# Kernel optimization log

Measured on AMD Instinct MI355X. Metric: run time of the kernel, lower is better.

Reference implementation:

```python
import jax, jax.numpy as jnp
import numpy as np

L = 2          # conv layers
N = 50000      # nodes
E = 800000     # edges (before self loops)
F_IN = 256     # raw node features
C = 32         # embed features (out_channels per head)
H = 4          # heads
HC = H * C
ED = 1         # edge feature dim
EPS = 1e-5
NEG_SLOPE = 0.2


def _xavier(k, shape):
    fan_in, fan_out = shape[-2], shape[-1]
    lim = float(np.sqrt(6.0 / (fan_in + fan_out)))
    return jax.random.uniform(k, shape, jnp.float32, -lim, lim)


def setup_inputs() -> dict:
    key = jax.random.key(0)
    ks = jax.random.split(key, 12)
    x = jax.random.normal(ks[0], (N, F_IN), jnp.float32)
    src = jax.random.randint(ks[1], (E,), 0, N, dtype=jnp.int32)
    off = jax.random.randint(ks[2], (E,), 1, N, dtype=jnp.int32)
    dst = (src + off) % N  # guarantees no pre-existing self loops (PyG removes then re-adds them)
    edge_index = jnp.stack([src, dst])
    edge_attr = jax.random.normal(ks[3], (E, ED), jnp.float32)
    return {
        "x": x,
        "edge_index": edge_index,
        "edge_attr": edge_attr,
        "W_emb": _xavier(ks[4], (F_IN, C)),
        "b_emb": jnp.zeros((C,), jnp.float32),
        "ln0_w": jnp.ones((C,), jnp.float32),
        "ln0_b": jnp.zeros((C,), jnp.float32),
        "Wl": _xavier(ks[5], (L, C, HC)),
        "bl": jnp.zeros((L, HC), jnp.float32),
        "Wr": _xavier(ks[6], (L, C, HC)),
        "br": jnp.zeros((L, HC), jnp.float32),
        "We": _xavier(ks[7], (L, ED, HC)),
        "att": jax.random.normal(ks[8], (L, H, C), jnp.float32) * 0.1,
        "gat_b": jnp.zeros((L, HC), jnp.float32),
        "ln1_w": jnp.ones((L, HC), jnp.float32),
        "ln1_b": jnp.zeros((L, HC), jnp.float32),
        "lin_w": _xavier(ks[9], (L, HC, C)),
        "lin_b": jnp.zeros((L, C), jnp.float32),
        "ln2_w": jnp.ones((L, C), jnp.float32),
        "ln2_b": jnp.zeros((L, C), jnp.float32),
    }


def _node_ln(x, w, b):
    # torch.nn.LayerNorm over last dim
    mu = jnp.mean(x, axis=-1, keepdims=True)
    xc = x - mu
    var = jnp.mean(xc * xc, axis=-1, keepdims=True)
    return xc / jnp.sqrt(var + EPS) * w + b


def _graph_ln(x, w, b):
    # torch_geometric.nn.norm.LayerNorm, mode='graph': normalize over ALL nodes+features
    mu = jnp.mean(x)
    xc = x - mu
    var = jnp.mean(xc * xc)
    return xc / jnp.sqrt(var + EPS) * w + b


def _gatv2_layer(h, src, dst, ea, Wl, bl, Wr, br, We, att, gat_b):
    n = h.shape[0]
    xl = (h @ Wl + bl).reshape(n, H, C)   # lin_l(x) -> source transform
    xr = (h @ Wr + br).reshape(n, H, C)   # lin_r(x) -> target transform
    e = (ea @ We).reshape(-1, H, C)       # lin_edge(edge_attr), no bias
    z = jax.nn.leaky_relu(xl[src] + xr[dst] + e, NEG_SLOPE)   # [Etot,H,C]
    logits = jnp.einsum("ehc,hc->eh", z, att)                  # [Etot,H]
    # segment softmax over destination nodes (every node has a self loop)
    m = jax.ops.segment_max(logits, dst, num_segments=n)
    ex = jnp.exp(logits - m[dst])
    s = jax.ops.segment_sum(ex, dst, num_segments=n)
    alpha = ex / s[dst]                                        # [Etot,H]
    msg = alpha[..., None] * xl[src]                           # [Etot,H,C]
    out = jax.ops.segment_sum(msg, dst, num_segments=n)        # [N,H,C]
    return out.reshape(n, HC) + gat_b


def reference(x, edge_index, edge_attr, W_emb, b_emb, ln0_w, ln0_b, Wl, bl, Wr, br,
              We, att, gat_b, ln1_w, ln1_b, lin_w, lin_b, ln2_w, ln2_b):
    n = x.shape[0]
    loop = jnp.arange(n, dtype=edge_index.dtype)
    src = jnp.concatenate([edge_index[0], loop])
    dst = jnp.concatenate([edge_index[1], loop])
    ea = jnp.concatenate([edge_attr, jnp.zeros((n, edge_attr.shape[1]), edge_attr.dtype)])  # fill_value=0.0

    # node_embed: Dropout(eval=identity) -> Linear -> LayerNorm -> ReLU
    h = jax.nn.relu(_node_ln(x @ W_emb + b_emb, ln0_w, ln0_b))
    hs = [h]
    for i in range(L):
        g = _gatv2_layer(h, src, dst, ea, Wl[i], bl[i], Wr[i], br[i], We[i], att[i], gat_b[i])
        g = jax.nn.relu(_graph_ln(g, ln1_w[i], ln1_b[i]))     # PyG graph-mode LayerNorm + ReLU
        g = g @ lin_w[i] + lin_b[i]                            # heads>1 projection back to C
        h = jax.nn.relu(_node_ln(g, ln2_w[i], ln2_b[i]))
        hs.append(h)
    # JumpingKnowledge mode='max': elementwise max over layer outputs
    return jnp.max(jnp.stack(hs, axis=0), axis=0)
```

## Files before the change

### kernel.cpp

```cpp
#include <hip/hip_runtime.h>
#include <hip/hip_fp16.h>

constexpr int kNodes = 50000;
constexpr int kNE    = 800000;
constexpr int kFin   = 256;
constexpr int kC     = 32;
constexpr int kH     = 4;
constexpr int kHC    = 128;
constexpr int kTN    = 16;
constexpr int kLWP   = 130;
constexpr int kEmbedBlocks = kNodes / kTN;
constexpr int kTransBlocks = (kNodes + 31) / 32;
constexpr int kHistGS = 256;
constexpr int kReoGS  = 256;
constexpr float kEps   = 1e-5f;
constexpr float kSlope = 0.2f;
constexpr float kL2E   = 1.44269504f;
constexpr float kShift2 = 8.0f * 1.44269504f;

typedef _Float16 f16;
typedef _Float16 f16x2 __attribute__((ext_vector_type(2)));
struct alignas(16) h8 { f16x2 v[4]; };

__device__ __forceinline__ float fdot2_(f16x2 a, f16x2 b, float c) {
#if __has_builtin(__builtin_amdgcn_fdot2)
    return __builtin_amdgcn_fdot2(a, b, c, false);
#else
    return fmaf((float)a.x, (float)b.x, fmaf((float)a.y, (float)b.y, c));
#endif
}

template<int CTRL>
__device__ __forceinline__ float dpp_add(float v) {
    int x = __builtin_amdgcn_update_dpp(0, __float_as_int(v), CTRL, 0xF, 0xF, true);
    return v + __int_as_float(x);
}
__device__ __forceinline__ float red8(float p) {
    p = dpp_add<0xB1>(p);
    p = dpp_add<0x4E>(p);
    p = dpp_add<0x141>(p);
    return p;
}

__global__ void __launch_bounds__(256) k_fill0(unsigned* __restrict__ p, int n) {
    int i = blockIdx.x * 256 + threadIdx.x;
    if (i < n) p[i] = 0u;
}

__global__ void __launch_bounds__(256) k_embed_hist(
    const float* __restrict__ x, const float* __restrict__ W, const float* __restrict__ b,
    const float* __restrict__ lnw, const float* __restrict__ lnb,
    float* __restrict__ h, float* __restrict__ jk,
    const int* __restrict__ dst, int* __restrict__ deg, unsigned short* __restrict__ rank) {
    __shared__ f16 sxh[kTN * kFin];
    __shared__ f16 sWh[kFin / 8 * kC * 8];
    int t = threadIdx.x;
    if (blockIdx.x < kHistGS) {
        const int stride = kHistGS * 256;
        int e = blockIdx.x * 256 + t;
        for (; e + 3 * stride < kNE; e += 4 * stride) {
            int d0 = dst[e], d1 = dst[e + stride], d2 = dst[e + 2 * stride], d3 = dst[e + 3 * stride];
            int r0 = atomicAdd(&deg[d0], 1);
            int r1 = atomicAdd(&deg[d1], 1);
            int r2 = atomicAdd(&deg[d2], 1);
            int r3 = atomicAdd(&deg[d3], 1);
            rank[e] = (unsigned short)r0;
            rank[e + stride] = (unsigned short)r1;
            rank[e + 2 * stride] = (unsigned short)r2;
            rank[e + 3 * stride] = (unsigned short)r3;
        }
        for (; e < kNE; e += stride) {
            int d = dst[e];
            rank[e] = (unsigned short)atomicAdd(&deg[d], 1);
        }
        return;
    }
    int n0 = (blockIdx.x - kHistGS) * kTN;
    for (int i = t; i < kFin * kC; i += 256) {
        int k = i >> 5, c = i & 31;
        sWh[((k >> 3) * kC + c) * 8 + (k & 7)] = (f16)W[i];
    }
    const float2* xg2 = (const float2*)(x + (long)n0 * kFin);
    f16x2* sx2 = (f16x2*)sxh;
    for (int i = t; i < kTN * kFin / 2; i += 256) {
        float2 v = xg2[i];
        f16x2 hv; hv.x = (f16)v.x; hv.y = (f16)v.y;
        sx2[i] = hv;
    }
    __syncthreads();
    int c = t & 31, n2 = t >> 5;
    const h8* xa = (const h8*)(sxh + n2 * kFin);
    const h8* xb = (const h8*)(sxh + (n2 + 8) * kFin);
    const h8* wr = (const h8*)sWh;
    float a0 = 0.f, a0b = 0.f, a1 = 0.f, a1b = 0.f;
    #pragma unroll 8
    for (int i8 = 0; i8 < kFin / 8; ++i8) {
        h8 xv0 = xa[i8];
        h8 xv1 = xb[i8];
        h8 wv  = wr[i8 * kC + c];
        a0  = fdot2_(xv0.v[0], wv.v[0], a0);
        a0b = fdot2_(xv0.v[1], wv.v[1], a0b);
        a0  = fdot2_(xv0.v[2], wv.v[2], a0);
        a0b = fdot2_(xv0.v[3], wv.v[3], a0b);
        a1  = fdot2_(xv1.v[0], wv.v[0], a1);
        a1b = fdot2_(xv1.v[1], wv.v[1], a1b);
        a1  = fdot2_(xv1.v[2], wv.v[2], a1);
        a1b = fdot2_(xv1.v[3], wv.v[3], a1b);
    }
    float acc0 = a0 + a0b, acc1 = a1 + a1b;
    float bc = b[c], lw = lnw[c], lb = lnb[c];
    {
        float y = acc0 + bc;
        float m = y;
        #pragma unroll
        for (int o = 1; o < 32; o <<= 1) m += __shfl_xor(m, o);
        m *= (1.f / kC);
        float xc = y - m, v = xc * xc;
        #pragma unroll
        for (int o = 1; o < 32; o <<= 1) v += __shfl_xor(v, o);
        v *= (1.f / kC);
        float out = fmaxf(xc * rsqrtf(v + kEps) * lw + lb, 0.f);
        int node = n0 + n2;
        h[node * kC + c] = out;
        jk[node * kC + c] = out;
    }
    {
        float y = acc1 + bc;
        float m = y;
        #pragma unroll
        for (int o = 1; o < 32; o <<= 1) m += __shfl_xor(m, o);
        m *= (1.f / kC);
        float xc = y - m, v = xc * xc;
        #pragma unroll
        for (int o = 1; o < 32; o <<= 1) v += __shfl_xor(v, o);
        v *= (1.f / kC);
        float out = fmaxf(xc * rsqrtf(v + kEps) * lw + lb, 0.f);
        int node = n0 + n2 + 8;
        h[node * kC + c] = out;
        jk[node * kC + c] = out;
    }
}

__device__ __forceinline__ void trans_body(
    int bid, float* s_h, const float* __restrict__ h,
    const float* __restrict__ Wl, const float* __restrict__ bl,
    const float* __restrict__ Wr, const float* __restrict__ br,
    __half* __restrict__ xl, float* __restrict__ xr) {
    int t = threadIdx.x;
    int j = t & 127, hf = t >> 7;
    float wl[kC], wr[kC];
    #pragma unroll
    for (int k = 0; k < kC; ++k) { wl[k] = Wl[k * kHC + j]; wr[k] = Wr[k * kHC + j]; }
    float blj = bl[j], brj = br[j];
    int n0 = bid * 32;
    int nn = min(32, kNodes - n0);
    for (int i = t; i < nn * kC; i += 256) s_h[i] = h[n0 * kC + i];
    __syncthreads();
    int nend = min(nn, hf * 16 + 16);
    for (int n = hf * 16; n < nend; ++n) {
        const float4* h4 = (const float4*)(s_h + n * kC);
        float al = blj, ar = brj;
        #pragma unroll
        for (int kq = 0; kq < 8; ++kq) {
            float4 hv = h4[kq];
            al += hv.x * wl[kq*4] + hv.y * wl[kq*4+1] + hv.z * wl[kq*4+2] + hv.w * wl[kq*4+3];
            ar += hv.x * wr[kq*4] + hv.y * wr[kq*4+1] + hv.z * wr[kq*4+2] + hv.w * wr[kq*4+3];
        }
        long g = (long)(n0 + n) * kHC + j;
        xl[g] = __float2half(al);
        xr[g] = ar;
    }
}

__global__ void __launch_bounds__(256) k_trans(
    const float* __restrict__ h,
    const float* __restrict__ Wl, const float* __restrict__ bl,
    const float* __restrict__ Wr, const float* __restrict__ br,
    __half* __restrict__ xl, float* __restrict__ xr) {
    __shared__ float s_h[32 * kC];
    trans_body(blockIdx.x, s_h, h, Wl, bl, Wr, br, xl, xr);
}

__global__ void __launch_bounds__(256) k_trans_reorder(
    const float* __restrict__ h,
    const float* __restrict__ Wl, const float* __restrict__ bl,
    const float* __restrict__ Wr, const float* __restrict__ br,
    __half* __restrict__ xl, float* __restrict__ xr,
    const int* __restrict__ src, const int* __restrict__ dst, const float* __restrict__ ea,
    const int* __restrict__ rowptr, const unsigned short* __restrict__ rank,
    int2* __restrict__ epack) {
    __shared__ float s_h[32 * kC];
    if (blockIdx.x < kReoGS) {
        const int stride = kReoGS * 256;
        int e = blockIdx.x * 256 + threadIdx.x;
        for (; e + 3 * stride < kNE; e += 4 * stride) {
            int e1 = e + stride, e2 = e + 2 * stride, e3 = e + 3 * stride;
            int d0 = dst[e], d1 = dst[e1], d2 = dst[e2], d3 = dst[e3];
            int r0 = rank[e], r1 = rank[e1], r2 = rank[e2], r3 = rank[e3];
            int p0 = rowptr[d0] + r0, p1 = rowptr[d1] + r1;
            int p2 = rowptr[d2] + r2, p3 = rowptr[d3] + r3;
            epack[p0] = make_int2(src[e],  __float_as_int(ea[e]));
            epack[p1] = make_int2(src[e1], __float_as_int(ea[e1]));
            epack[p2] = make_int2(src[e2], __float_as_int(ea[e2]));
            epack[p3] = make_int2(src[e3], __float_as_int(ea[e3]));
        }
        for (; e < kNE; e += stride) {
            int d = dst[e];
            int pos = rowptr[d] + (int)rank[e];
            epack[pos] = make_int2(src[e], __float_as_int(ea[e]));
        }
        return;
    }
    trans_body(blockIdx.x - kReoGS, s_h, h, Wl, bl, Wr, br, xl, xr);
}

__global__ void __launch_bounds__(256) k_scan1(const int* __restrict__ deg,
                                               int* __restrict__ excl, int* __restrict__ bsum) {
    __shared__ int s[256];
    int t = threadIdx.x;
    int i = blockIdx.x * 256 + t;
    int v = (i < kNodes) ? deg[i] : 0;
    s[t] = v;
    __syncthreads();
    for (int o = 1; o < 256; o <<= 1) {
        int tv = (t >= o) ? s[t - o] : 0;
        __syncthreads();
        s[t] += tv;
        __syncthreads();
    }
    if (i < kNodes) excl[i] = s[t] - v;
    if (t == 255) bsum[blockIdx.x] = s[255];
}

__global__ void __launch_bounds__(256) k_scan2(int* __restrict__ bsum, int nb) {
    __shared__ int s[256];
    int t = threadIdx.x;
    int v = (t < nb) ? bsum[t] : 0;
    s[t] = v;
    __syncthreads();
    for (int o = 1; o < 256; o <<= 1) {
        int tv = (t >= o) ? s[t - o] : 0;
        __syncthreads();
        s[t] += tv;
        __syncthreads();
    }
    if (t < nb) bsum[t] = s[t];
}

__global__ void __launch_bounds__(256) k_scan3(int* __restrict__ excl, const int* __restrict__ bsum) {
    int i = blockIdx.x * 256 + threadIdx.x;
    if (i >= kNodes) return;
    if (blockIdx.x > 0) excl[i] += bsum[blockIdx.x - 1];
}

__global__ void __launch_bounds__(256) k_edge(
    const int* __restrict__ rowptr, const int* __restrict__ deg,
    const int2* __restrict__ epack,
    const __half* __restrict__ xl, float* __restrict__ xrg,
    const float* __restrict__ We, const float* __restrict__ att,
    const float* __restrict__ gat_b, float* __restrict__ ps, float* __restrict__ pq) {
    struct h4 { __half2 a, b; };
    int t = threadIdx.x & 63;
    int w = __builtin_amdgcn_readfirstlane(threadIdx.x >> 6);
    int d = blockIdx.x * 4 + w;
    int f = t & 31;
    bool slot0 = (t < 32);
    float em0 = slot0 ? 1.f : 0.f;

    const h4* xl4 = (const h4*)xl;
    long rowq = (long)d * 32;

    float4 xrv = ((const float4*)xrg)[rowq + f];
    float4 Wev = ((const float4*)We)[f];
    float4 av  = ((const float4*)att)[f];
    av.x *= kL2E; av.y *= kL2E; av.z *= kL2E; av.w *= kL2E;
    float4 gb  = ((const float4*)gat_b)[f];

    h4 xs = xl4[rowq + f];
    float2 xs01 = __half22float2(xs.a), xs23 = __half22float2(xs.b);

    float z0 = xs01.x + xrv.x, z1 = xs01.y + xrv.y;
    float z2 = xs23.x + xrv.z, z3 = xs23.y + xrv.w;
    z0 = fmaxf(z0, kSlope * z0); z1 = fmaxf(z1, kSlope * z1);
    z2 = fmaxf(z2, kSlope * z2); z3 = fmaxf(z3, kSlope * z3);
    float p = red8(z0 * av.x + z1 * av.y + z2 * av.z + z3 * av.w);
    float ee = __builtin_amdgcn_exp2f(p - kShift2) * em0;
    float l = ee;
    float o0 = ee * xs01.x, o1 = ee * xs01.y, o2 = ee * xs23.x, o3 = ee * xs23.y;

    int base = rowptr[d], cnt = deg[d];
    int npair = cnt >> 1;
    int e = 0;
    for (; e + 4 <= npair; e += 4) {
        int2 pa[4], pb[4];
        #pragma unroll
        for (int u = 0; u < 4; ++u) {
            pa[u] = epack[base + 2 * (e + u)];
            pb[u] = epack[base + 2 * (e + u) + 1];
        }
        h4 xv[4]; float eav[4];
        #pragma unroll
        for (int u = 0; u < 4; ++u) {
            int srow = slot0 ? pa[u].x : pb[u].x;
            xv[u] = xl4[(long)srow * 32 + f];
            eav[u] = __int_as_float(slot0 ? pa[u].y : pb[u].y);
        }
        #pragma unroll
        for (int u = 0; u < 4; ++u) {
            float2 x01 = __half22float2(xv[u].a), x23 = __half22float2(xv[u].b);
            float a0 = fmaf(eav[u], Wev.x, xrv.x) + x01.x;
            float a1 = fmaf(eav[u], Wev.y, xrv.y) + x01.y;
            float a2 = fmaf(eav[u], Wev.z, xrv.z) + x23.x;
            float a3 = fmaf(eav[u], Wev.w, xrv.w) + x23.y;
            a0 = fmaxf(a0, kSlope * a0); a1 = fmaxf(a1, kSlope * a1);
            a2 = fmaxf(a2, kSlope * a2); a3 = fmaxf(a3, kSlope * a3);
            float pp = red8(a0 * av.x + a1 * av.y + a2 * av.z + a3 * av.w);
            float eu = __builtin_amdgcn_exp2f(pp - kShift2);
            l += eu;
            o0 = fmaf(eu, x01.x, o0); o1 = fmaf(eu, x01.y, o1);
            o2 = fmaf(eu, x23.x, o2); o3 = fmaf(eu, x23.y, o3);
        }
    }
    for (; e < npair; ++e) {
        int2 pa = epack[base + 2 * e];
        int2 pb = epack[base + 2 * e + 1];
        int srow = slot0 ? pa.x : pb.x;
        float eav = __int_as_float(slot0 ? pa.y : pb.y);
        h4 xv = xl4[(long)srow * 32 + f];
        float2 x01 = __half22float2(xv.a), x23 = __half22float2(xv.b);
        float a0 = fmaf(eav, Wev.x, xrv.x) + x01.x;
        float a1 = fmaf(eav, Wev.y, xrv.y) + x01.y;
        float a2 = fmaf(eav, Wev.z, xrv.z) + x23.x;
        float a3 = fmaf(eav, Wev.w, xrv.w) + x23.y;
        a0 = fmaxf(a0, kSlope * a0); a1 = fmaxf(a1, kSlope * a1);
        a2 = fmaxf(a2, kSlope * a2); a3 = fmaxf(a3, kSlope * a3);
        float pp = red8(a0 * av.x + a1 * av.y + a2 * av.z + a3 * av.w);
        float eu = __builtin_amdgcn_exp2f(pp - kShift2);
        l += eu;
        o0 = fmaf(eu, x01.x, o0); o1 = fmaf(eu, x01.y, o1);
        o2 = fmaf(eu, x23.x, o2); o3 = fmaf(eu, x23.y, o3);
    }
    if (cnt & 1) {
        int2 ep = epack[base + cnt - 1];
        int srow = ep.x;
        float eav = __int_as_float(ep.y);
        h4 xv = xl4[(long)srow * 32 + f];
        float2 x01 = __half22float2(xv.a), x23 = __half22float2(xv.b);
        float a0 = fmaf(eav, Wev.x, xrv.x) + x01.x;
        float a1 = fmaf(eav, Wev.y, xrv.y) + x01.y;
        float a2 = fmaf(eav, Wev.z, xrv.z) + x23.x;
        float a3 = fmaf(eav, Wev.w, xrv.w) + x23.y;
        a0 = fmaxf(a0, kSlope * a0); a1 = fmaxf(a1, kSlope * a1);
        a2 = fmaxf(a2, kSlope * a2); a3 = fmaxf(a3, kSlope * a3);
        float pp = red8(a0 * av.x + a1 * av.y + a2 * av.z + a3 * av.w);
        float eu = __builtin_amdgcn_exp2f(pp - kShift2) * em0;
        l += eu;
        o0 = fmaf(eu, x01.x, o0); o1 = fmaf(eu, x01.y, o1);
        o2 = fmaf(eu, x23.x, o2); o3 = fmaf(eu, x23.y, o3);
    }
    l  += __shfl_xor(l, 32);
    o0 += __shfl_xor(o0, 32); o1 += __shfl_xor(o1, 32);
    o2 += __shfl_xor(o2, 32); o3 += __shfl_xor(o3, 32);
    float rl = __builtin_amdgcn_rcpf(l);
    float v0 = o0 * rl, v1 = o1 * rl, v2 = o2 * rl, v3 = o3 * rl;
    if (slot0)
        ((float4*)xrg)[rowq + f] = make_float4(v0, v1, v2, v3);
    float vb0 = v0 + gb.x, vb1 = v1 + gb.y, vb2 = v2 + gb.z, vb3 = v3 + gb.w;
    float s = vb0 + vb1 + vb2 + vb3;
    float q = vb0 * vb0 + vb1 * vb1 + vb2 * vb2 + vb3 * vb3;
    #pragma unroll
    for (int mm = 1; mm < 32; mm <<= 1) { s += __shfl_xor(s, mm); q += __shfl_xor(q, mm); }
    if (t == 0) { ps[d] = s; pq[d] = q; }
}

__global__ void __launch_bounds__(1024) k_statsr(
    const float* __restrict__ ps, const float* __restrict__ pq, float* __restrict__ stats) {
    __shared__ float rs[1024], rq[1024];
    int t = threadIdx.x;
    float s = 0.f, q = 0.f;
    for (int i = t; i < kNodes; i += 1024) { s += ps[i]; q += pq[i]; }
    rs[t] = s; rq[t] = q;
    __syncthreads();
    for (int o = 512; o > 0; o >>= 1) {
        if (t < o) { rs[t] += rs[t + o]; rq[t] += rq[t + o]; }
        __syncthreads();
    }
    if (t == 0) { stats[0] = rs[0]; stats[1] = rq[0]; }
}

__global__ void __launch_bounds__(256) k_post(
    const float* __restrict__ g, const float* __restrict__ gat_b,
    const float* __restrict__ ln1w, const float* __restrict__ ln1b,
    const float* __restrict__ linw, const float* __restrict__ linb,
    const float* __restrict__ ln2w, const float* __restrict__ ln2b,
    const float* __restrict__ stats, const float* __restrict__ jk_in,
    float* __restrict__ h, float* __restrict__ jk_out) {
    __shared__ float s_lwT[kC * kLWP];
    __shared__ float s_vb[8 * kHC];
    int t = threadIdx.x;
    int n0 = blockIdx.x * 8;
    const float inv = 1.f / ((float)kNodes * kHC);
    float mean = stats[0] * inv;
    float var  = stats[1] * inv - mean * mean;
    float rstd = rsqrtf(var + kEps);
    for (int i = t; i < kHC * kC; i += 256) {
        int k = i >> 5, c = i & 31;
        s_lwT[c * kLWP + k] = linw[i];
    }
    for (int i = t; i < 8 * kHC; i += 256) {
        int node = n0 + (i >> 7), f = i & 127;
        float a = (g[(long)node * kHC + f] + gat_b[f] - mean) * rstd * ln1w[f] + ln1b[f];
        s_vb[i] = fmaxf(a, 0.f);
    }
    __syncthreads();
    int n = t >> 5, c = t & 31;
    int node = n0 + n;
    float acc = linb[c];
    const float* vb = s_vb + n * kHC;
    const float* wr = s_lwT + c * kLWP;
    #pragma unroll 8
    for (int k = 0; k < kHC; k += 4) {
        float4 v4 = *(const float4*)(vb + k);
        float2 w0 = *(const float2*)(wr + k);
        float2 w1 = *(const float2*)(wr + k + 2);
        acc += v4.x * w0.x + v4.y * w0.y + v4.z * w1.x + v4.w * w1.y;
    }
    float m = acc;
    #pragma unroll
    for (int mm = 1; mm < 32; mm <<= 1) m += __shfl_xor(m, mm);
    m *= (1.f / kC);
    float dd = acc - m;
    float q = dd * dd;
    #pragma unroll
    for (int mm = 1; mm < 32; mm <<= 1) q += __shfl_xor(q, mm);
    q *= (1.f / kC);
    float out = dd * rsqrtf(q + kEps) * ln2w[c] + ln2b[c];
    out = fmaxf(out, 0.f);
    h[node * kC + c] = out;
    jk_out[node * kC + c] = fmaxf(jk_in[node * kC + c], out);
}

extern "C" void kernel_launch(void* const* d_in, const int* in_sizes, int n_in,
                              void* d_out, int out_size, void* d_ws, size_t ws_size,
                              hipStream_t stream) {
    (void)in_sizes; (void)n_in; (void)out_size; (void)ws_size;
    const float* x     = (const float*)d_in[0];
    const int*   ei    = (const int*)d_in[1];
    const int*   src   = ei;
    const int*   dst   = ei + kNE;
    const float* ea    = (const float*)d_in[2];
    const float* W_emb = (const float*)d_in[3];
    const float* b_emb = (const float*)d_in[4];
    const float* ln0w  = (const float*)d_in[5];
    const float* ln0b  = (const float*)d_in[6];
    const float* Wl    = (const float*)d_in[7];
    const float* bl    = (const float*)d_in[8];
    const float* Wr    = (const float*)d_in[9];
    const float* br    = (const float*)d_in[10];
    const float* We    = (const float*)d_in[11];
    const float* att   = (const float*)d_in[12];
    const float* gat_b = (const float*)d_in[13];
    const float* ln1w  = (const float*)d_in[14];
    const float* ln1b  = (const float*)d_in[15];
    const float* linw  = (const float*)d_in[16];
    const float* linb  = (const float*)d_in[17];
    const float* ln2w  = (const float*)d_in[18];
    const float* ln2b  = (const float*)d_in[19];

    char* wsb = (char*)d_ws;
    float*  h      = (float*)(wsb);
    float*  jk     = (float*)(wsb +  6400000);
    float*  xrg    = (float*)(wsb + 12800000);
    __half* xl     = (__half*)(wsb + 38400000);
    int2*   epack  = (int2*)(wsb + 51200000);
    int*    deg    = (int*)(wsb + 57600000);
    int*    rowptr = (int*)(wsb + 58000000);
    int*    bsum   = (int*)(wsb + 58200000);
    float*  stats  = (float*)(wsb + 58201024);
    float*  ps     = (float*)(wsb + 58300000);
    float*  pq     = (float*)(wsb + 58500000);
    unsigned short* rank = (unsigned short*)(wsb + 58700000);

    const int scanBlocks = (kNodes + 255) / 256;
    const int edgeBlocks = kNodes / 4;
    const int postBlocks = kNodes / 8;

    hipLaunchKernelGGL(k_fill0, dim3((kNodes + 255) / 256), dim3(256), 0, stream,
                       (unsigned*)deg, kNodes);
    hipLaunchKernelGGL(k_embed_hist, dim3(kHistGS + kEmbedBlocks), dim3(256), 0, stream,
                       x, W_emb, b_emb, ln0w, ln0b, h, jk, dst, deg, rank);
    hipLaunchKernelGGL(k_scan1, dim3(scanBlocks), dim3(256), 0, stream, deg, rowptr, bsum);
    hipLaunchKernelGGL(k_scan2, dim3(1), dim3(256), 0, stream, bsum, scanBlocks);
    hipLaunchKernelGGL(k_scan3, dim3(scanBlocks), dim3(256), 0, stream, rowptr, bsum);
    hipLaunchKernelGGL(k_trans_reorder, dim3(kReoGS + kTransBlocks), dim3(256), 0, stream,
                       h, Wl, bl, Wr, br, xl, xrg,
                       src, dst, ea, rowptr, rank, epack);
    for (int l = 0; l < 2; ++l) {
        if (l == 1) {
            hipLaunchKernelGGL(k_trans, dim3(kTransBlocks), dim3(256), 0, stream,
                               h, Wl + l * kC * kHC, bl + l * kHC,
                               Wr + l * kC * kHC, br + l * kHC, xl, xrg);
        }
        hipLaunchKernelGGL(k_edge, dim3(edgeBlocks), dim3(256), 0, stream,
                           rowptr, deg, epack, xl, xrg,
                           We + l * kHC, att + l * kH * kC, gat_b + l * kHC, ps, pq);
        hipLaunchKernelGGL(k_statsr, dim3(1), dim3(1024), 0, stream, ps, pq, stats);
        hipLaunchKernelGGL(k_post, dim3(postBlocks), dim3(256), 0, stream,
                           xrg, gat_b + l * kHC, ln1w + l * kHC, ln1b + l * kHC,
                           linw + l * kHC * kC, linb + l * kC,
                           ln2w + l * kC, ln2b + l * kC, stats, jk,
                           h, (l == 1) ? (float*)d_out : jk);
    }
}
```

Before: 419.3 us.

## Precompute fp16 embed weights, unroll edge loop by 8, parallelize stats reduction

Converts the embedding weight to a pre-swizzled fp16 buffer once in a prep kernel fused with the degree clear, so each embed block copies it instead of converting it. The GAT edge loop is factored into a templated batch helper with an 8-way unrolled main loop to raise memory-level parallelism on the gathers. The global stats reduction now uses 8 blocks with atomic adds, with stats zeroed in the preceding trans kernel. This adds extra registers in the edge kernel and makes the float summation order nondeterministic.

```diff
diff --git a/kernel.cpp b/kernel.cpp
--- a/kernel.cpp
+++ b/kernel.cpp
@@ -13,6 +13,7 @@
 constexpr int kTransBlocks = (kNodes + 31) / 32;
 constexpr int kHistGS = 256;
 constexpr int kReoGS  = 256;
+constexpr int kDegBlocks = (kNodes + 255) / 256;
 constexpr float kEps   = 1e-5f;
 constexpr float kSlope = 0.2f;
 constexpr float kL2E   = 1.44269504f;
@@ -42,13 +43,21 @@
     return p;
 }
 
-__global__ void __launch_bounds__(256) k_fill0(unsigned* __restrict__ p, int n) {
-    int i = blockIdx.x * 256 + threadIdx.x;
-    if (i < n) p[i] = 0u;
+__global__ void __launch_bounds__(256) k_prep(
+    unsigned* __restrict__ deg, const float* __restrict__ W, f16* __restrict__ Wh) {
+    int t = threadIdx.x;
+    if (blockIdx.x < kDegBlocks) {
+        int i = blockIdx.x * 256 + t;
+        if (i < kNodes) deg[i] = 0u;
+        return;
+    }
+    int i = (blockIdx.x - kDegBlocks) * 256 + t;
+    int k = i >> 5, c = i & 31;
+    Wh[((k >> 3) * kC + c) * 8 + (k & 7)] = (f16)W[i];
 }
 
 __global__ void __launch_bounds__(256) k_embed_hist(
-    const float* __restrict__ x, const float* __restrict__ W, const float* __restrict__ b,
+    const float* __restrict__ x, const f16* __restrict__ Wh, const float* __restrict__ b,
     const float* __restrict__ lnw, const float* __restrict__ lnb,
     float* __restrict__ h, float* __restrict__ jk,
     const int* __restrict__ dst, int* __restrict__ deg, unsigned short* __restrict__ rank) {
@@ -76,9 +85,10 @@
         return;
     }
     int n0 = (blockIdx.x - kHistGS) * kTN;
-    for (int i = t; i < kFin * kC; i += 256) {
-        int k = i >> 5, c = i & 31;
-        sWh[((k >> 3) * kC + c) * 8 + (k & 7)] = (f16)W[i];
+    {
+        const h8* Wg = (const h8*)Wh;
+        h8* sW8 = (h8*)sWh;
+        for (int i = t; i < kFin * kC / 8; i += 256) sW8[i] = Wg[i];
     }
     const float2* xg2 = (const float2*)(x + (long)n0 * kFin);
     f16x2* sx2 = (f16x2*)sxh;
@@ -176,8 +186,9 @@
     const float* __restrict__ h,
     const float* __restrict__ Wl, const float* __restrict__ bl,
     const float* __restrict__ Wr, const float* __restrict__ br,
-    __half* __restrict__ xl, float* __restrict__ xr) {
+    __half* __restrict__ xl, float* __restrict__ xr, float* __restrict__ stats) {
     __shared__ float s_h[32 * kC];
+    if (blockIdx.x == 0 && threadIdx.x == 0) { stats[0] = 0.f; stats[1] = 0.f; }
     trans_body(blockIdx.x, s_h, h, Wl, bl, Wr, br, xl, xr);
 }
 
@@ -188,7 +199,7 @@
     __half* __restrict__ xl, float* __restrict__ xr,
     const int* __restrict__ src, const int* __restrict__ dst, const float* __restrict__ ea,
     const int* __restrict__ rowptr, const unsigned short* __restrict__ rank,
-    int2* __restrict__ epack) {
+    int2* __restrict__ epack, float* __restrict__ stats) {
     __shared__ float s_h[32 * kC];
     if (blockIdx.x < kReoGS) {
         const int stride = kReoGS * 256;
@@ -211,6 +222,7 @@
         }
         return;
     }
+    if (blockIdx.x == kReoGS && threadIdx.x == 0) { stats[0] = 0.f; stats[1] = 0.f; }
     trans_body(blockIdx.x - kReoGS, s_h, h, Wl, bl, Wr, br, xl, xr);
 }
 
@@ -253,13 +265,48 @@
     if (blockIdx.x > 0) excl[i] += bsum[blockIdx.x - 1];
 }
 
+struct h4 { __half2 a, b; };
+template<int U>
+__device__ __forceinline__ void gat_batch(
+    const int2* __restrict__ epack, int base2, bool slot0, int f,
+    const h4* __restrict__ xl4, float4 Wev, float4 xrv, float4 av,
+    float& l, float& o0, float& o1, float& o2, float& o3) {
+    int2 pa[U], pb[U];
+    #pragma unroll
+    for (int u = 0; u < U; ++u) {
+        pa[u] = epack[base2 + 2 * u];
+        pb[u] = epack[base2 + 2 * u + 1];
+    }
+    h4 xv[U]; float eav[U];
+    #pragma unroll
+    for (int u = 0; u < U; ++u) {
+        int srow = slot0 ? pa[u].x : pb[u].x;
+        xv[u] = xl4[(long)srow * 32 + f];
+        eav[u] = __int_as_float(slot0 ? pa[u].y : pb[u].y);
+    }
+    #pragma unroll
+    for (int u = 0; u < U; ++u) {
+        float2 x01 = __half22float2(xv[u].a), x23 = __half22float2(xv[u].b);
+        float a0 = fmaf(eav[u], Wev.x, xrv.x) + x01.x;
+        float a1 = fmaf(eav[u], Wev.y, xrv.y) + x01.y;
+        float a2 = fmaf(eav[u], Wev.z, xrv.z) + x23.x;
+        float a3 = fmaf(eav[u], Wev.w, xrv.w) + x23.y;
+        a0 = fmaxf(a0, kSlope * a0); a1 = fmaxf(a1, kSlope * a1);
+        a2 = fmaxf(a2, kSlope * a2); a3 = fmaxf(a3, kSlope * a3);
+        float pp = red8(a0 * av.x + a1 * av.y + a2 * av.z + a3 * av.w);
+        float eu = __builtin_amdgcn_exp2f(pp - kShift2);
+        l += eu;
+        o0 = fmaf(eu, x01.x, o0); o1 = fmaf(eu, x01.y, o1);
+        o2 = fmaf(eu, x23.x, o2); o3 = fmaf(eu, x23.y, o3);
+    }
+}
+
 __global__ void __launch_bounds__(256) k_edge(
     const int* __restrict__ rowptr, const int* __restrict__ deg,
     const int2* __restrict__ epack,
     const __half* __restrict__ xl, float* __restrict__ xrg,
     const float* __restrict__ We, const float* __restrict__ att,
     const float* __restrict__ gat_b, float* __restrict__ ps, float* __restrict__ pq) {
-    struct h4 { __half2 a, b; };
     int t = threadIdx.x & 63;
     int w = __builtin_amdgcn_readfirstlane(threadIdx.x >> 6);
     int d = blockIdx.x * 4 + w;
@@ -291,55 +338,14 @@
     int base = rowptr[d], cnt = deg[d];
     int npair = cnt >> 1;
     int e = 0;
-    for (; e + 4 <= npair; e += 4) {
-        int2 pa[4], pb[4];
-        #pragma unroll
-        for (int u = 0; u < 4; ++u) {
-            pa[u] = epack[base + 2 * (e + u)];
-            pb[u] = epack[base + 2 * (e + u) + 1];
-        }
-        h4 xv[4]; float eav[4];
-        #pragma unroll
-        for (int u = 0; u < 4; ++u) {
-            int srow = slot0 ? pa[u].x : pb[u].x;
-            xv[u] = xl4[(long)srow * 32 + f];
-            eav[u] = __int_as_float(slot0 ? pa[u].y : pb[u].y);
-        }
-        #pragma unroll
-        for (int u = 0; u < 4; ++u) {
-            float2 x01 = __half22float2(xv[u].a), x23 = __half22float2(xv[u].b);
-            float a0 = fmaf(eav[u], Wev.x, xrv.x) + x01.x;
-            float a1 = fmaf(eav[u], Wev.y, xrv.y) + x01.y;
-            float a2 = fmaf(eav[u], Wev.z, xrv.z) + x23.x;
-            float a3 = fmaf(eav[u], Wev.w, xrv.w) + x23.y;
-            a0 = fmaxf(a0, kSlope * a0); a1 = fmaxf(a1, kSlope * a1);
-            a2 = fmaxf(a2, kSlope * a2); a3 = fmaxf(a3, kSlope * a3);
-            float pp = red8(a0 * av.x + a1 * av.y + a2 * av.z + a3 * av.w);
-            float eu = __builtin_amdgcn_exp2f(pp - kShift2);
-            l += eu;
-            o0 = fmaf(eu, x01.x, o0); o1 = fmaf(eu, x01.y, o1);
-            o2 = fmaf(eu, x23.x, o2); o3 = fmaf(eu, x23.y, o3);
-        }
-    }
-    for (; e < npair; ++e) {
-        int2 pa = epack[base + 2 * e];
-        int2 pb = epack[base + 2 * e + 1];
-        int srow = slot0 ? pa.x : pb.x;
-        float eav = __int_as_float(slot0 ? pa.y : pb.y);
-        h4 xv = xl4[(long)srow * 32 + f];
-        float2 x01 = __half22float2(xv.a), x23 = __half22float2(xv.b);
-        float a0 = fmaf(eav, Wev.x, xrv.x) + x01.x;
-        float a1 = fmaf(eav, Wev.y, xrv.y) + x01.y;
-        float a2 = fmaf(eav, Wev.z, xrv.z) + x23.x;
-        float a3 = fmaf(eav, Wev.w, xrv.w) + x23.y;
-        a0 = fmaxf(a0, kSlope * a0); a1 = fmaxf(a1, kSlope * a1);
-        a2 = fmaxf(a2, kSlope * a2); a3 = fmaxf(a3, kSlope * a3);
-        float pp = red8(a0 * av.x + a1 * av.y + a2 * av.z + a3 * av.w);
-        float eu = __builtin_amdgcn_exp2f(pp - kShift2);
-        l += eu;
-        o0 = fmaf(eu, x01.x, o0); o1 = fmaf(eu, x01.y, o1);
-        o2 = fmaf(eu, x23.x, o2); o3 = fmaf(eu, x23.y, o3);
-    }
+    for (; e + 8 <= npair; e += 8)
+        gat_batch<8>(epack, base + 2 * e, slot0, f, xl4, Wev, xrv, av, l, o0, o1, o2, o3);
+    if (e + 4 <= npair) {
+        gat_batch<4>(epack, base + 2 * e, slot0, f, xl4, Wev, xrv, av, l, o0, o1, o2, o3);
+        e += 4;
+    }
+    for (; e < npair; ++e)
+        gat_batch<1>(epack, base + 2 * e, slot0, f, xl4, Wev, xrv, av, l, o0, o1, o2, o3);
     if (cnt & 1) {
         int2 ep = epack[base + cnt - 1];
         int srow = ep.x;
@@ -378,14 +384,14 @@
     __shared__ float rs[1024], rq[1024];
     int t = threadIdx.x;
     float s = 0.f, q = 0.f;
-    for (int i = t; i < kNodes; i += 1024) { s += ps[i]; q += pq[i]; }
+    for (int i = blockIdx.x * 1024 + t; i < kNodes; i += 8 * 1024) { s += ps[i]; q += pq[i]; }
     rs[t] = s; rq[t] = q;
     __syncthreads();
     for (int o = 512; o > 0; o >>= 1) {
         if (t < o) { rs[t] += rs[t + o]; rq[t] += rq[t + o]; }
         __syncthreads();
     }
-    if (t == 0) { stats[0] = rs[0]; stats[1] = rq[0]; }
+    if (t == 0) { atomicAdd(&stats[0], rs[0]); atomicAdd(&stats[1], rq[0]); }
 }
 
 __global__ void __launch_bounds__(256) k_post(
@@ -480,31 +486,32 @@
     float*  ps     = (float*)(wsb + 58300000);
     float*  pq     = (float*)(wsb + 58500000);
     unsigned short* rank = (unsigned short*)(wsb + 58700000);
+    f16*    Wh     = (f16*)(wsb + 60400000);
 
     const int scanBlocks = (kNodes + 255) / 256;
     const int edgeBlocks = kNodes / 4;
     const int postBlocks = kNodes / 8;
 
-    hipLaunchKernelGGL(k_fill0, dim3((kNodes + 255) / 256), dim3(256), 0, stream,
-                       (unsigned*)deg, kNodes);
+    hipLaunchKernelGGL(k_prep, dim3(kDegBlocks + 32), dim3(256), 0, stream,
+                       (unsigned*)deg, W_emb, Wh);
     hipLaunchKernelGGL(k_embed_hist, dim3(kHistGS + kEmbedBlocks), dim3(256), 0, stream,
-                       x, W_emb, b_emb, ln0w, ln0b, h, jk, dst, deg, rank);
+                       x, Wh, b_emb, ln0w, ln0b, h, jk, dst, deg, rank);
     hipLaunchKernelGGL(k_scan1, dim3(scanBlocks), dim3(256), 0, stream, deg, rowptr, bsum);
     hipLaunchKernelGGL(k_scan2, dim3(1), dim3(256), 0, stream, bsum, scanBlocks);
     hipLaunchKernelGGL(k_scan3, dim3(scanBlocks), dim3(256), 0, stream, rowptr, bsum);
     hipLaunchKernelGGL(k_trans_reorder, dim3(kReoGS + kTransBlocks), dim3(256), 0, stream,
                        h, Wl, bl, Wr, br, xl, xrg,
-                       src, dst, ea, rowptr, rank, epack);
+                       src, dst, ea, rowptr, rank, epack, stats);
     for (int l = 0; l < 2; ++l) {
         if (l == 1) {
             hipLaunchKernelGGL(k_trans, dim3(kTransBlocks), dim3(256), 0, stream,
                                h, Wl + l * kC * kHC, bl + l * kHC,
-                               Wr + l * kC * kHC, br + l * kHC, xl, xrg);
+                               Wr + l * kC * kHC, br + l * kHC, xl, xrg, stats);
         }
         hipLaunchKernelGGL(k_edge, dim3(edgeBlocks), dim3(256), 0, stream,
                            rowptr, deg, epack, xl, xrg,
                            We + l * kHC, att + l * kH * kC, gat_b + l * kHC, ps, pq);
-        hipLaunchKernelGGL(k_statsr, dim3(1), dim3(1024), 0, stream, ps, pq, stats);
+        hipLaunchKernelGGL(k_statsr, dim3(8), dim3(1024), 0, stream, ps, pq, stats);
         hipLaunchKernelGGL(k_post, dim3(postBlocks), dim3(256), 0, stream,
                            xrg, gat_b + l * kHC, ln1w + l * kHC, ln1b + l * kHC,
                            linw + l * kHC * kC, linb + l * kC,
```

Result: no change. 418.9 us (-0.1%).
